# Kernel optimization log

Measured on AMD Instinct MI355X. Metric: run time of the kernel, lower is better.

## Reference

```python
import jax, jax.numpy as jnp
import numpy as np

C_IN, C_OUT, K, PAD, STRIDE = 128, 256, 3, 1, 1
H = W = 256


def setup_inputs() -> dict:
    key = jax.random.key(0)
    k1, k2, k3 = jax.random.split(key, 3)
    # batch=1: the original forward uses X_pad[0] for every batch index,
    # so with m=1 the buggy loop and a standard conv are mathematically identical.
    x = jax.random.normal(k1, (1, C_IN, H, W), dtype=jnp.float32)
    # nn.Parameter(torch.rand(...)) -> uniform[0,1)
    weight = jax.random.uniform(k2, (C_OUT, C_IN, K, K), dtype=jnp.float32)
    bias = jax.random.uniform(k3, (C_OUT,), dtype=jnp.float32)
    return {"x": x, "weight": weight, "bias": bias}


def reference(x, weight, bias):
    # Faithful math of convAppx.forward with FP_appx_mul treated as exact
    # multiply (FP_appx_mul is not defined in the source): a plain 2D
    # cross-correlation (no kernel flip, matching the sliced elementwise
    # product) with symmetric padding, stride 1, plus per-channel bias.
    z = jax.lax.conv_general_dilated(
        x, weight,
        window_strides=(STRIDE, STRIDE),
        padding=((PAD, PAD), (PAD, PAD)),
        dimension_numbers=("NCHW", "OIHW", "NCHW"),
    )
    return z + bias[None, :, None, None]
```

## Files before the change

kernel.cpp:

```cpp
#include <hip/hip_runtime.h>
#include <hip/hip_bf16.h>


typedef short bf16x8 __attribute__((ext_vector_type(8)));
typedef float f32x4 __attribute__((ext_vector_type(4)));
typedef int   i32x4 __attribute__((ext_vector_type(4)));
typedef unsigned short u16x4 __attribute__((ext_vector_type(4)));
typedef unsigned short u16x8 __attribute__((ext_vector_type(8)));

#define CIN   128
#define COUT  256
#define HH    256
#define WW    256
#define HP    258
#define ROWP  (HP * CIN)

static __device__ __forceinline__ unsigned short f2bf(float v) {
    __hip_bfloat16 b = __float2bfloat16(v);
    return *reinterpret_cast<unsigned short*>(&b);
}

static __device__ __forceinline__ void gload_lds16(const unsigned short* g, unsigned short* l) {
    __builtin_amdgcn_global_load_lds(
        (const __attribute__((address_space(1))) unsigned int*)g,
        (__attribute__((address_space(3))) unsigned int*)l, 16, 0, 0);
}

template<int CTRL>
static __device__ __forceinline__ bf16x8 rotf(bf16x8 a) {
    i32x4 ai = __builtin_bit_cast(i32x4, a);
    i32x4 r;
    #pragma unroll
    for (int j = 0; j < 4; ++j)
        r[j] = __builtin_amdgcn_mov_dpp(ai[j], CTRL, 0xF, 0xF, true);
    return __builtin_bit_cast(bf16x8, r);
}
#define ROR_P1 0x12F
#define ROR_P2 0x12E

__global__ __launch_bounds__(256) void prep_kernel(const float* __restrict__ x,
                                                   const float* __restrict__ w,
                                                   unsigned short* __restrict__ xb,
                                                   unsigned short* __restrict__ wr) {
    int bid = blockIdx.x;
    int t   = threadIdx.x;

    if (bid < 65) {
        int i = bid * 256 + t;
        if (i < 16448) {
            u16x8 z = {0, 0, 0, 0, 0, 0, 0, 0};
            int off;
            if (i < 8256) {
                int r   = (i >= 4128) ? 1 : 0;
                int rem = i - r * 4128;
                off = (r * 257) * ROWP + rem * 8;
            } else {
                int j   = i - 8256;
                int col = j >> 12;
                int rem = j & 4095;
                int hp  = (rem >> 4) + 1;
                int c8  = rem & 15;
                off = hp * ROWP + (col * 257) * CIN + c8 * 8;
            }
            *(u16x8*)(&xb[off]) = z;
        }
    }

    if (bid < 128) {
        int p = bid * 256 + t;
        const float* src = w + p * 9;
        #pragma unroll
        for (int khw = 0; khw < 9; ++khw)
            wr[khw * (COUT * CIN) + p] = f2bf(src[khw]);
    }

    int h  = bid >> 2;
    int w0 = (bid & 3) * 64;
    __shared__ unsigned short tile[CIN * 72];

    int wq  = t & 15;
    int cib = t >> 4;
    for (int c0 = 0; c0 < CIN; c0 += 16) {
        int ci = c0 + cib;
        float4 v = *(const float4*)(x + ci * (HH * WW) + h * WW + w0 + wq * 4);
        u16x4 p;
        p.x = f2bf(v.x); p.y = f2bf(v.y); p.z = f2bf(v.z); p.w = f2bf(v.w);
        *(u16x4*)(&tile[ci * 72 + wq * 4]) = p;
    }
    __syncthreads();

    for (int it = 0; it < 4; ++it) {
        int idx = it * 256 + t;
        int ww_ = idx & 63;
        int c8  = idx >> 6;
        u16x8 o;
        #pragma unroll
        for (int j = 0; j < 8; ++j)
            o[j] = tile[(c8 * 8 + j) * 72 + ww_];
        int dst = ((h + 1) * HP + (w0 + ww_ + 1)) * CIN + c8 * 8;
        *(u16x8*)(&xb[dst]) = o;
    }
}

__global__ __launch_bounds__(256, 4) void conv_mfma_kernel(const unsigned short* __restrict__ xb,
                                                           const unsigned short* __restrict__ wr,
                                                           const float* __restrict__ bias,
                                                           float* __restrict__ out) {
    __shared__ unsigned short A0[128 * 32];
    __shared__ unsigned short A1[128 * 32];
    __shared__ unsigned short A2[128 * 32];
    __shared__ unsigned short Bs[130 * 32];

    int bid   = blockIdx.x;
    int inner = bid >> 3;
    int h     = (bid & 7) * 32 + (inner >> 2);
    int co0   = (inner & 1) * 128;
    int s0    = ((inner >> 1) & 1) * 128;

    int t    = threadIdx.x;
    int lane = t & 63;
    int wave = t >> 6;
    int quad = lane >> 4;
    int l16  = lane & 15;

    f32x4 acc[2][8];
    #pragma unroll
    for (int mi = 0; mi < 2; ++mi)
        #pragma unroll
        for (int ni = 0; ni < 8; ++ni)
            acc[mi][ni] = (f32x4){0.f, 0.f, 0.f, 0.f};

    #pragma unroll 1
    for (int i = 0; i < 12; ++i) {
        int kh  = i >> 2;
        int ciq = i & 3;

        {
            const unsigned short* wbase =
                wr + (size_t)(kh * 3) * (COUT * CIN) + co0 * CIN + ciq * 32;
            #pragma unroll
            for (int it = 0; it < 2; ++it) {
                int seg = it * 256 + t;
                int r   = seg >> 2;
                int s   = seg & 3;
                int c   = s ^ ((r >> 1) & 3);
                const unsigned short* src = wbase + r * CIN + c * 8;
                gload_lds16(src,                    &A0[seg * 8]);
                gload_lds16(src + (COUT * CIN),     &A1[seg * 8]);
                gload_lds16(src + 2 * (COUT * CIN), &A2[seg * 8]);
            }
        }
        {
            const unsigned short* xrow = xb + (size_t)(h + kh) * ROWP + ciq * 32;
            #pragma unroll
            for (int it = 0; it < 2; ++it) {
                int seg = it * 256 + t;
                int lc  = seg >> 2;
                int s   = seg & 3;
                int c   = s ^ ((lc >> 1) & 3);
                gload_lds16(xrow + (s0 + lc) * CIN + c * 8, &Bs[seg * 8]);
            }
            if (t < 8) {
                int seg = 512 + t;
                int lc  = seg >> 2;
                int s   = seg & 3;
                int c   = s ^ ((lc >> 1) & 3);
                gload_lds16(xrow + (s0 + lc) * CIN + c * 8, &Bs[seg * 8]);
            }
        }
        asm volatile("s_waitcnt vmcnt(0)" ::: "memory");
        __builtin_amdgcn_s_barrier();
        __builtin_amdgcn_sched_barrier(0);

        {
            int ck = quad;

            bf16x8 af0[2], af1[2], af2[2];
            #pragma unroll
            for (int mi = 0; mi < 2; ++mi) {
                int row = wave * 32 + mi * 16 + l16;
                int ro  = row * 32 + (ck ^ ((row >> 1) & 3)) * 8;
                af0[mi] = *(const bf16x8*)(&A0[ro]);
                af1[mi] = *(const bf16x8*)(&A1[ro]);
                af2[mi] = *(const bf16x8*)(&A2[ro]);
            }

            auto rdB = [&](int ni_) -> bf16x8 {
                int lc = ni_ * 16 + l16;
                if (lc > 129) lc = 129;
                return *(const bf16x8*)(&Bs[lc * 32 + ((ck ^ ((lc >> 1) & 3)) * 8)]);
            };

            bf16x8 cur = rdB(0);
            #pragma unroll
            for (int ni = 0; ni < 8; ++ni) {
                bf16x8 nxt = rdB(ni + 1);
                bf16x8 r1c = rotf<ROR_P1>(cur), r1n = rotf<ROR_P1>(nxt);
                bf16x8 s1  = (l16 == 15) ? r1n : r1c;
                bf16x8 r2c = rotf<ROR_P2>(cur), r2n = rotf<ROR_P2>(nxt);
                bf16x8 s2  = (l16 >= 14) ? r2n : r2c;

                __builtin_amdgcn_s_setprio(1);
                #pragma unroll
                for (int mi = 0; mi < 2; ++mi)
                    acc[mi][ni] = __builtin_amdgcn_mfma_f32_16x16x32_bf16(
                        af0[mi], cur, acc[mi][ni], 0, 0, 0);
                #pragma unroll
                for (int mi = 0; mi < 2; ++mi)
                    acc[mi][ni] = __builtin_amdgcn_mfma_f32_16x16x32_bf16(
                        af1[mi], s1, acc[mi][ni], 0, 0, 0);
                #pragma unroll
                for (int mi = 0; mi < 2; ++mi)
                    acc[mi][ni] = __builtin_amdgcn_mfma_f32_16x16x32_bf16(
                        af2[mi], s2, acc[mi][ni], 0, 0, 0);
                __builtin_amdgcn_s_setprio(0);
                cur = nxt;
            }
        }
        __builtin_amdgcn_s_barrier();
        __builtin_amdgcn_sched_barrier(0);
    }

    #pragma unroll
    for (int mi = 0; mi < 2; ++mi) {
        #pragma unroll
        for (int r = 0; r < 4; ++r) {
            int co = co0 + wave * 32 + mi * 16 + quad * 4 + r;
            float b = bias[co];
            float* orow = out + (size_t)co * (HH * WW) + h * WW + s0 + l16;
            #pragma unroll
            for (int ni = 0; ni < 8; ++ni)
                orow[ni * 16] = acc[mi][ni][r] + b;
        }
    }
}

extern "C" void kernel_launch(void* const* d_in, const int* in_sizes, int n_in,
                              void* d_out, int out_size, void* d_ws, size_t ws_size,
                              hipStream_t stream) {
    const float* x    = (const float*)d_in[0];
    const float* w    = (const float*)d_in[1];
    const float* bias = (const float*)d_in[2];
    float* out        = (float*)d_out;

    unsigned short* xb = (unsigned short*)d_ws;
    unsigned short* wr = xb + (size_t)HP * HP * CIN;

    prep_kernel<<<dim3(1024), dim3(256), 0, stream>>>(x, w, xb, wr);
    conv_mfma_kernel<<<dim3(1024), dim3(256), 0, stream>>>(xb, wr, bias, out);
}
```

Measured before the change: 139.5 us.

## Fuse input bf16 conversion and NHWC transpose into conv kernel

Removes the padded NHWC bf16 copy of the input that the prep kernel used to build. The conv kernel now reads fp32 NCHW rows directly, converts them to bf16 and transposes them through a shared-memory staging tile into a full-channel B buffer, and handles the zero padding inline. This saves the write and re-read of the intermediate activation buffer and shrinks the prep kernel to the weight conversion only. In exchange it adds conversion work and extra __syncthreads inside the conv kernel, raises LDS use, and lowers the occupancy hint from 4 to 2 blocks per CU. Each block also redoes the conversion for its input rows, so rows shared across blocks are converted several times.

```diff
diff --git a/kernel.cpp b/kernel.cpp
--- a/kernel.cpp
+++ b/kernel.cpp
@@ -12,8 +12,6 @@
 #define COUT  256
 #define HH    256
 #define WW    256
-#define HP    258
-#define ROWP  (HP * CIN)
 
 static __device__ __forceinline__ unsigned short f2bf(float v) {
     __hip_bfloat16 b = __float2bfloat16(v);
@@ -38,78 +36,24 @@
 #define ROR_P1 0x12F
 #define ROR_P2 0x12E
 
-__global__ __launch_bounds__(256) void prep_kernel(const float* __restrict__ x,
-                                                   const float* __restrict__ w,
-                                                   unsigned short* __restrict__ xb,
+__global__ __launch_bounds__(256) void prep_kernel(const float* __restrict__ w,
                                                    unsigned short* __restrict__ wr) {
-    int bid = blockIdx.x;
-    int t   = threadIdx.x;
-
-    if (bid < 65) {
-        int i = bid * 256 + t;
-        if (i < 16448) {
-            u16x8 z = {0, 0, 0, 0, 0, 0, 0, 0};
-            int off;
-            if (i < 8256) {
-                int r   = (i >= 4128) ? 1 : 0;
-                int rem = i - r * 4128;
-                off = (r * 257) * ROWP + rem * 8;
-            } else {
-                int j   = i - 8256;
-                int col = j >> 12;
-                int rem = j & 4095;
-                int hp  = (rem >> 4) + 1;
-                int c8  = rem & 15;
-                off = hp * ROWP + (col * 257) * CIN + c8 * 8;
-            }
-            *(u16x8*)(&xb[off]) = z;
-        }
-    }
-
-    if (bid < 128) {
-        int p = bid * 256 + t;
-        const float* src = w + p * 9;
-        #pragma unroll
-        for (int khw = 0; khw < 9; ++khw)
-            wr[khw * (COUT * CIN) + p] = f2bf(src[khw]);
-    }
-
-    int h  = bid >> 2;
-    int w0 = (bid & 3) * 64;
-    __shared__ unsigned short tile[CIN * 72];
-
-    int wq  = t & 15;
-    int cib = t >> 4;
-    for (int c0 = 0; c0 < CIN; c0 += 16) {
-        int ci = c0 + cib;
-        float4 v = *(const float4*)(x + ci * (HH * WW) + h * WW + w0 + wq * 4);
-        u16x4 p;
-        p.x = f2bf(v.x); p.y = f2bf(v.y); p.z = f2bf(v.z); p.w = f2bf(v.w);
-        *(u16x4*)(&tile[ci * 72 + wq * 4]) = p;
-    }
-    __syncthreads();
-
-    for (int it = 0; it < 4; ++it) {
-        int idx = it * 256 + t;
-        int ww_ = idx & 63;
-        int c8  = idx >> 6;
-        u16x8 o;
-        #pragma unroll
-        for (int j = 0; j < 8; ++j)
-            o[j] = tile[(c8 * 8 + j) * 72 + ww_];
-        int dst = ((h + 1) * HP + (w0 + ww_ + 1)) * CIN + c8 * 8;
-        *(u16x8*)(&xb[dst]) = o;
-    }
-}
-
-__global__ __launch_bounds__(256, 4) void conv_mfma_kernel(const unsigned short* __restrict__ xb,
+    int p = blockIdx.x * 256 + threadIdx.x;
+    const float* src = w + p * 9;
+    #pragma unroll
+    for (int khw = 0; khw < 9; ++khw)
+        wr[khw * (COUT * CIN) + p] = f2bf(src[khw]);
+}
+
+__global__ __launch_bounds__(256, 2) void conv_mfma_kernel(const float* __restrict__ x,
                                                            const unsigned short* __restrict__ wr,
                                                            const float* __restrict__ bias,
                                                            float* __restrict__ out) {
     __shared__ unsigned short A0[128 * 32];
     __shared__ unsigned short A1[128 * 32];
     __shared__ unsigned short A2[128 * 32];
-    __shared__ unsigned short Bs[130 * 32];
+    __shared__ unsigned short Bs[130 * 128];
+    __shared__ unsigned short Xs[32 * 132];
 
     int bid   = blockIdx.x;
     int inner = bid >> 3;
@@ -130,95 +74,137 @@
         for (int ni = 0; ni < 8; ++ni)
             acc[mi][ni] = (f32x4){0.f, 0.f, 0.f, 0.f};
 
+    auto stageA = [&](int kh_, int ciq_) {
+        const unsigned short* wbase =
+            wr + (size_t)(kh_ * 3) * (COUT * CIN) + co0 * CIN + ciq_ * 32;
+        #pragma unroll
+        for (int it = 0; it < 2; ++it) {
+            int seg = it * 256 + t;
+            int r   = seg >> 2;
+            int s   = seg & 3;
+            int c   = s ^ ((r >> 1) & 3);
+            const unsigned short* src = wbase + r * CIN + c * 8;
+            gload_lds16(src,                    &A0[seg * 8]);
+            gload_lds16(src + (COUT * CIN),     &A1[seg * 8]);
+            gload_lds16(src + 2 * (COUT * CIN), &A2[seg * 8]);
+        }
+    };
+
     #pragma unroll 1
-    for (int i = 0; i < 12; ++i) {
-        int kh  = i >> 2;
-        int ciq = i & 3;
-
-        {
-            const unsigned short* wbase =
-                wr + (size_t)(kh * 3) * (COUT * CIN) + co0 * CIN + ciq * 32;
+    for (int kh = 0; kh < 3; ++kh) {
+        int row = h + kh - 1;
+
+        stageA(kh, 0);
+
+        if (row >= 0 && row < HH) {
+            #pragma unroll 1
+            for (int cic = 0; cic < 4; ++cic) {
+                const float* xbase = x + (size_t)(cic * 32) * (HH * WW) + (size_t)row * WW + s0;
+                #pragma unroll
+                for (int it = 0; it < 4; ++it) {
+                    int seg = it * 256 + t;
+                    int ci  = seg >> 5;
+                    int f4i = seg & 31;
+                    float4 v = *(const float4*)(xbase + (size_t)ci * (HH * WW) + f4i * 4);
+                    u16x4 pk;
+                    pk.x = f2bf(v.x); pk.y = f2bf(v.y); pk.z = f2bf(v.z); pk.w = f2bf(v.w);
+                    *(u16x4*)(&Xs[ci * 132 + f4i * 4]) = pk;
+                }
+                if (t < 64) {
+                    int ci   = t >> 1;
+                    int side = t & 1;
+                    int gw   = s0 - 1 + side * 129;
+                    float vv = (gw >= 0 && gw < WW)
+                        ? x[(size_t)(cic * 32 + ci) * (HH * WW) + (size_t)row * WW + gw] : 0.f;
+                    Xs[ci * 132 + 129 - side] = f2bf(vv);
+                }
+                __syncthreads();
+                #pragma unroll
+                for (int it = 0; it < 3; ++it) {
+                    int seg = it * 256 + t;
+                    if (seg < 520) {
+                        int lc  = seg >> 2;
+                        int sub = seg & 3;
+                        int xc  = (lc == 0) ? 129 : (lc - 1);
+                        u16x8 o;
+                        #pragma unroll
+                        for (int j = 0; j < 8; ++j)
+                            o[j] = Xs[(sub * 8 + j) * 132 + xc];
+                        int cg = cic * 4 + sub;
+                        *(u16x8*)(&Bs[lc * 128 + ((cg ^ (lc & 15)) * 8)]) = o;
+                    }
+                }
+                __syncthreads();
+            }
+        } else {
+            u16x8 z = {0, 0, 0, 0, 0, 0, 0, 0};
             #pragma unroll
-            for (int it = 0; it < 2; ++it) {
+            for (int it = 0; it < 9; ++it) {
                 int seg = it * 256 + t;
-                int r   = seg >> 2;
-                int s   = seg & 3;
-                int c   = s ^ ((r >> 1) & 3);
-                const unsigned short* src = wbase + r * CIN + c * 8;
-                gload_lds16(src,                    &A0[seg * 8]);
-                gload_lds16(src + (COUT * CIN),     &A1[seg * 8]);
-                gload_lds16(src + 2 * (COUT * CIN), &A2[seg * 8]);
-            }
-        }
-        {
-            const unsigned short* xrow = xb + (size_t)(h + kh) * ROWP + ciq * 32;
-            #pragma unroll
-            for (int it = 0; it < 2; ++it) {
-                int seg = it * 256 + t;
-                int lc  = seg >> 2;
-                int s   = seg & 3;
-                int c   = s ^ ((lc >> 1) & 3);
-                gload_lds16(xrow + (s0 + lc) * CIN + c * 8, &Bs[seg * 8]);
-            }
-            if (t < 8) {
-                int seg = 512 + t;
-                int lc  = seg >> 2;
-                int s   = seg & 3;
-                int c   = s ^ ((lc >> 1) & 3);
-                gload_lds16(xrow + (s0 + lc) * CIN + c * 8, &Bs[seg * 8]);
-            }
-        }
-        asm volatile("s_waitcnt vmcnt(0)" ::: "memory");
-        __builtin_amdgcn_s_barrier();
-        __builtin_amdgcn_sched_barrier(0);
-
-        {
-            int ck = quad;
-
-            bf16x8 af0[2], af1[2], af2[2];
-            #pragma unroll
-            for (int mi = 0; mi < 2; ++mi) {
-                int row = wave * 32 + mi * 16 + l16;
-                int ro  = row * 32 + (ck ^ ((row >> 1) & 3)) * 8;
-                af0[mi] = *(const bf16x8*)(&A0[ro]);
-                af1[mi] = *(const bf16x8*)(&A1[ro]);
-                af2[mi] = *(const bf16x8*)(&A2[ro]);
-            }
-
-            auto rdB = [&](int ni_) -> bf16x8 {
-                int lc = ni_ * 16 + l16;
-                if (lc > 129) lc = 129;
-                return *(const bf16x8*)(&Bs[lc * 32 + ((ck ^ ((lc >> 1) & 3)) * 8)]);
-            };
-
-            bf16x8 cur = rdB(0);
-            #pragma unroll
-            for (int ni = 0; ni < 8; ++ni) {
-                bf16x8 nxt = rdB(ni + 1);
-                bf16x8 r1c = rotf<ROR_P1>(cur), r1n = rotf<ROR_P1>(nxt);
-                bf16x8 s1  = (l16 == 15) ? r1n : r1c;
-                bf16x8 r2c = rotf<ROR_P2>(cur), r2n = rotf<ROR_P2>(nxt);
-                bf16x8 s2  = (l16 >= 14) ? r2n : r2c;
-
-                __builtin_amdgcn_s_setprio(1);
-                #pragma unroll
-                for (int mi = 0; mi < 2; ++mi)
-                    acc[mi][ni] = __builtin_amdgcn_mfma_f32_16x16x32_bf16(
-                        af0[mi], cur, acc[mi][ni], 0, 0, 0);
-                #pragma unroll
-                for (int mi = 0; mi < 2; ++mi)
-                    acc[mi][ni] = __builtin_amdgcn_mfma_f32_16x16x32_bf16(
-                        af1[mi], s1, acc[mi][ni], 0, 0, 0);
-                #pragma unroll
-                for (int mi = 0; mi < 2; ++mi)
-                    acc[mi][ni] = __builtin_amdgcn_mfma_f32_16x16x32_bf16(
-                        af2[mi], s2, acc[mi][ni], 0, 0, 0);
-                __builtin_amdgcn_s_setprio(0);
-                cur = nxt;
-            }
-        }
-        __builtin_amdgcn_s_barrier();
-        __builtin_amdgcn_sched_barrier(0);
+                if (seg < 2080) *(u16x8*)(&Bs[seg * 8]) = z;
+            }
+            __syncthreads();
+        }
+
+        #pragma unroll 1
+        for (int ciq = 0; ciq < 4; ++ciq) {
+            if (ciq > 0) {
+                __builtin_amdgcn_s_barrier();
+                stageA(kh, ciq);
+            }
+            asm volatile("s_waitcnt vmcnt(0)" ::: "memory");
+            __builtin_amdgcn_s_barrier();
+            __builtin_amdgcn_sched_barrier(0);
+
+            {
+                int ck = quad;
+                int cb = ciq * 4 + quad;
+
+                bf16x8 af0[2], af1[2], af2[2];
+                #pragma unroll
+                for (int mi = 0; mi < 2; ++mi) {
+                    int r  = wave * 32 + mi * 16 + l16;
+                    int ro = r * 32 + (ck ^ ((r >> 1) & 3)) * 8;
+                    af0[mi] = *(const bf16x8*)(&A0[ro]);
+                    af1[mi] = *(const bf16x8*)(&A1[ro]);
+                    af2[mi] = *(const bf16x8*)(&A2[ro]);
+                }
+
+                auto rdB = [&](int ni_) -> bf16x8 {
+                    int lc = ni_ * 16 + l16;
+                    if (lc > 129) lc = 129;
+                    return *(const bf16x8*)(&Bs[lc * 128 + ((cb ^ (lc & 15)) * 8)]);
+                };
+
+                bf16x8 cur = rdB(0);
+                #pragma unroll
+                for (int ni = 0; ni < 8; ++ni) {
+                    bf16x8 nxt = rdB(ni + 1);
+                    bf16x8 r1c = rotf<ROR_P1>(cur), r1n = rotf<ROR_P1>(nxt);
+                    bf16x8 s1  = (l16 == 15) ? r1n : r1c;
+                    bf16x8 r2c = rotf<ROR_P2>(cur), r2n = rotf<ROR_P2>(nxt);
+                    bf16x8 s2  = (l16 >= 14) ? r2n : r2c;
+
+                    __builtin_amdgcn_s_setprio(1);
+                    #pragma unroll
+                    for (int mi = 0; mi < 2; ++mi)
+                        acc[mi][ni] = __builtin_amdgcn_mfma_f32_16x16x32_bf16(
+                            af0[mi], cur, acc[mi][ni], 0, 0, 0);
+                    #pragma unroll
+                    for (int mi = 0; mi < 2; ++mi)
+                        acc[mi][ni] = __builtin_amdgcn_mfma_f32_16x16x32_bf16(
+                            af1[mi], s1, acc[mi][ni], 0, 0, 0);
+                    #pragma unroll
+                    for (int mi = 0; mi < 2; ++mi)
+                        acc[mi][ni] = __builtin_amdgcn_mfma_f32_16x16x32_bf16(
+                            af2[mi], s2, acc[mi][ni], 0, 0, 0);
+                    __builtin_amdgcn_s_setprio(0);
+                    cur = nxt;
+                }
+            }
+            __builtin_amdgcn_s_barrier();
+            __builtin_amdgcn_sched_barrier(0);
+        }
     }
 
     #pragma unroll
@@ -243,9 +229,8 @@
     const float* bias = (const float*)d_in[2];
     float* out        = (float*)d_out;
 
-    unsigned short* xb = (unsigned short*)d_ws;
-    unsigned short* wr = xb + (size_t)HP * HP * CIN;
-
-    prep_kernel<<<dim3(1024), dim3(256), 0, stream>>>(x, w, xb, wr);
-    conv_mfma_kernel<<<dim3(1024), dim3(256), 0, stream>>>(xb, wr, bias, out);
-}
+    unsigned short* wr = (unsigned short*)d_ws;
+
+    prep_kernel<<<dim3(128), dim3(256), 0, stream>>>(w, wr);
+    conv_mfma_kernel<<<dim3(1024), dim3(256), 0, stream>>>(x, wr, bias, out);
+}
```

Measured after the change: 159.3 us. 14.2% more time.
